# Optimization experiments

Measured on AMD Instinct MI355X. Metric: run time of the kernel, lower is better.

Reference implementation:

```python
import jax, jax.numpy as jnp
import numpy as np

NFEAT, NHID, NCLASS = 64, 64, 32
B, N_SOLUTE, N_SOLVENT = 2, 2076, 8940


def setup_inputs() -> dict:
    key = jax.random.key(0)
    ks = jax.random.split(key, 20)
    s = 0.05
    return {
        "solute_adj": jax.random.uniform(ks[0], (B, N_SOLUTE, N_SOLUTE), jnp.float32),
        "solute_meth": jax.random.normal(ks[1], (B, N_SOLUTE, NFEAT), jnp.float32),
        "solvent_meth": jax.random.normal(ks[2], (B, N_SOLVENT, NFEAT), jnp.float32),
        "solvent_adj_meth": jax.random.uniform(ks[3], (B, N_SOLVENT, N_SOLVENT), jnp.float32),
        "W_fc1": jax.random.normal(ks[4], (NFEAT, NCLASS), jnp.float32) * s,
        "b_fc1": jnp.zeros((NCLASS,), jnp.float32),
        "W_c1": jax.random.normal(ks[5], (NFEAT, NHID), jnp.float32) * s,
        "b_c1": jnp.zeros((NHID,), jnp.float32),
        "W_c2": jax.random.normal(ks[6], (NHID, NCLASS), jnp.float32) * s,
        "b_c2": jnp.zeros((NCLASS,), jnp.float32),
        "W_fc2": jax.random.normal(ks[7], (2 * NCLASS, NCLASS), jnp.float32) * s,
        "b_fc2": jnp.zeros((NCLASS,), jnp.float32),
        "W_fc3": jax.random.normal(ks[8], (NCLASS, 64), jnp.float32) * s,
        "b_fc3": jnp.zeros((64,), jnp.float32),
        "W_fc4": jax.random.normal(ks[9], (64, 32), jnp.float32) * s,
        "b_fc4": jnp.zeros((32,), jnp.float32),
        "W_fc5": jax.random.normal(ks[10], (32, 1), jnp.float32) * s,
        "b_fc5": jnp.zeros((1,), jnp.float32),
    }


def _branch(x, adj, W_fc1, b_fc1, W_c1, b_c1, W_c2, b_c2):
    # residual linear skip: fc1(x)
    init = x @ W_fc1 + b_fc1                          # [B, N, nclass]
    # GCNConv 1: adj @ (x W) + b, relu
    h = jax.nn.relu(jnp.einsum("bnm,bmh->bnh", adj, x @ W_c1) + b_c1)
    # GCNConv 2 + skip
    out = jnp.einsum("bnm,bmc->bnc", adj, h @ W_c2) + b_c2 + init  # [B, N, nclass]
    # global max pool: batch index is block-contiguous -> max over node axis
    return jnp.max(out, axis=1)                       # [B, nclass]


def reference(solute_adj, solute_meth, solvent_meth, solvent_adj_meth,
              W_fc1, b_fc1, W_c1, b_c1, W_c2, b_c2,
              W_fc2, b_fc2, W_fc3, b_fc3, W_fc4, b_fc4, W_fc5, b_fc5):
    su = _branch(solute_meth, solute_adj, W_fc1, b_fc1, W_c1, b_c1, W_c2, b_c2)
    sv = _branch(solvent_meth, solvent_adj_meth, W_fc1, b_fc1, W_c1, b_c1, W_c2, b_c2)
    d = jnp.concatenate([su, sv], axis=1)             # [B, 2*nclass]
    d = jax.nn.relu(d @ W_fc2 + b_fc2)                # dropout = identity (eval)
    d = jax.nn.relu(d @ W_fc3 + b_fc3)
    d = jax.nn.relu(d @ W_fc4 + b_fc4)
    return d @ W_fc5 + b_fc5                          # [B, 1]
```

## Files before the change

### kernel.cpp

```cpp
#include <hip/hip_runtime.h>

#define B_      2
#define NSU     2076
#define NSV     8940
#define ROWS_SU (B_ * NSU)
#define ROWS_ALL (B_ * (NSU + NSV))
#define MP_SU   2176
#define MP_SV   8960
#define NB64_SV 140
#define NB64_SU 33
#define NBX_TOT (2 * NB64_SV + 2 * NB64_SU)
#define NH1     5
#define NH2     8
#define KQ_SV   1792
#define KQ_SU   448
#define NCH_SV  140
#define NCH_SU  33
#define T_SV    560
#define T_SU    132
#define TILES_TOT (2 * T_SV + 2 * T_SU)
#define PADROWS (TILES_TOT * 16)
#define TSZ8_SV ((size_t)140 * 1024)
#define TSZ8_SU ((size_t)34 * 1024)
#define SU_BASE8 ((size_t)2 * T_SV * TSZ8_SV)
#define NEG_INF (-3.402823466e38f)

#define Y1F_SV(b) ((size_t)(b) * 140 * 4096)
#define Y1F_SU(b) ((size_t)2 * 140 * 4096 + (size_t)(b) * 34 * 4096)
#define Y2F8_SV(b) ((size_t)(b) * 140 * 2048)
#define Y2F8_SU(b) ((size_t)2 * 140 * 2048 + (size_t)(b) * 34 * 2048)

typedef __attribute__((ext_vector_type(8))) short bf16x8;
typedef __attribute__((ext_vector_type(4))) float f32x4;
typedef __attribute__((ext_vector_type(2))) long longx2;

union BF8 { bf16x8 v; unsigned int u[4]; };

#define MFMA16 __builtin_amdgcn_mfma_f32_16x16x32_bf16
#define MFMA8  __builtin_amdgcn_mfma_f32_16x16x32_fp8_fp8

__device__ __forceinline__ unsigned short f2bf(float x) {
    unsigned int u = __float_as_uint(x);
    u += 0x7FFFu + ((u >> 16) & 1u);
    return (unsigned short)(u >> 16);
}
__device__ __forceinline__ unsigned int pkbf(float lo, float hi) {
    unsigned int r;
    asm("v_cvt_pk_bf16_f32 %0, %1, %2" : "=v"(r) : "v"(lo), "v"(hi));
    return r;
}
__device__ __forceinline__ int pk8lo(float lo, float hi, int old) {
    return __builtin_amdgcn_cvt_pk_fp8_f32(lo, hi, old, false);
}
__device__ __forceinline__ int pk8hi(float lo, float hi, int old) {
    return __builtin_amdgcn_cvt_pk_fp8_f32(lo, hi, old, true);
}

__global__ __launch_bounds__(256) void pre_kernel(
    const float* __restrict__ xsu, const float* __restrict__ xsv,
    const float* __restrict__ Wc1, const float* __restrict__ Wfc1,
    const float* __restrict__ bfc1,
    unsigned short* __restrict__ y1tf, float* __restrict__ initb)
{
    __shared__ float sWc1[64 * 64];
    __shared__ float sWfc1[64 * 32];
    __shared__ float sb[32];
    const int tid = threadIdx.x;
    for (int i = tid; i < 64 * 64; i += 256) sWc1[i] = Wc1[i];
    for (int i = tid; i < 64 * 32; i += 256) sWfc1[i] = Wfc1[i];
    if (tid < 32) sb[tid] = bfc1[tid];
    __syncthreads();

    const int rid = blockIdx.x * 256 + tid;
    if (rid >= ROWS_ALL) return;

    const float* xrow; unsigned short* yb; int m;
    if (rid < ROWS_SU) {
        int b = rid / NSU; m = rid - b * NSU;
        xrow = xsu + (size_t)rid * 64;
        yb = y1tf + Y1F_SU(b);
    } else {
        int r2 = rid - ROWS_SU;
        int b = r2 / NSV; m = r2 - b * NSV;
        xrow = xsv + (size_t)r2 * 64;
        yb = y1tf + Y1F_SV(b);
    }

    float xr[64];
    #pragma unroll
    for (int f4 = 0; f4 < 16; ++f4) {
        float4 v = ((const float4*)xrow)[f4];
        xr[f4 * 4 + 0] = v.x; xr[f4 * 4 + 1] = v.y;
        xr[f4 * 4 + 2] = v.z; xr[f4 * 4 + 3] = v.w;
    }
    {
        const int chunk = m >> 6, half = (m >> 5) & 1, kqq = (m >> 3) & 3, e = m & 7;
        unsigned short* yw = yb + (size_t)chunk * 4096 + half * 512 + e;
        for (int c = 0; c < 64; ++c) {
            float acc = 0.f;
            #pragma unroll
            for (int f = 0; f < 64; ++f) acc += xr[f] * sWc1[f * 64 + c];
            yw[(c >> 4) * 1024 + ((c & 15) + 16 * kqq) * 8] = f2bf(acc);
        }
    }
    float* ini = initb + (size_t)rid * 32;
    for (int c = 0; c < 32; ++c) {
        float acc = sb[c];
        #pragma unroll
        for (int f = 0; f < 64; ++f) acc += xr[f] * sWfc1[f * 32 + c];
        ini[c] = acc;
    }
}

__global__ __launch_bounds__(256) void conv1p_kernel(
    const float* __restrict__ adj_su, const float* __restrict__ adj_sv,
    const unsigned short* __restrict__ y1tf,
    unsigned char* __restrict__ abf8,
    float* __restrict__ p1)
{
    const int bid = blockIdx.x;
    const int q = blockIdx.y;
    const int tid = threadIdx.x, lane = tid & 63, wid = tid >> 6;
    int M, row0, tile0, KQ;
    const float* A; const unsigned short* Yf; unsigned char* AbT;
    if (bid < 2 * NB64_SV) {
        int b = bid / NB64_SV, rb = bid - b * NB64_SV;
        M = NSV; KQ = KQ_SV;
        A  = adj_sv + (size_t)b * NSV * NSV;
        Yf = y1tf + Y1F_SV(b);
        row0 = rb * 64; tile0 = b * T_SV + rb * 4;
        AbT = abf8 + (size_t)(tile0 + wid) * TSZ8_SV;
    } else {
        int t = bid - 2 * NB64_SV;
        int b = t / NB64_SU, rb = t - b * NB64_SU;
        M = NSU; KQ = KQ_SU;
        A  = adj_su + (size_t)b * NSU * NSU;
        Yf = y1tf + Y1F_SU(b);
        row0 = rb * 64;
        int tsu = b * T_SU + rb * 4;
        tile0 = 2 * T_SV + tsu;
        AbT = abf8 + SU_BASE8 + (size_t)(tsu + wid) * TSZ8_SU;
    }
    const int kbeg = q * KQ;
    const int kend = (q == NH1 - 1) ? M : (kbeg + KQ);

    const int l15 = lane & 15, kq = lane >> 4;
    const int gr  = row0 + wid * 16 + l15;
    const int grc = (gr < M) ? gr : (M - 1);
    const float* Ap  = A + (size_t)grc * M;
    const float* Apk = Ap + kq * 8;
    const unsigned short* Bl = Yf + (size_t)lane * 8;

    f32x4 acc0 = {0.f,0.f,0.f,0.f}, acc1 = acc0, acc2 = acc0, acc3 = acc0;

    float4 a0,a1,a2,a3, c0,c1,c2,c3;
    bf16x8 b0,b1,b2,b3,b4,b5,b6,b7, d0,d1,d2,d3,d4,d5,d6,d7;

#define LDA(A0,A1,A2,A3,kc) do { \
    A0 = *(const float4*)(Apk + (kc)); \
    A1 = *(const float4*)(Apk + (kc) + 4); \
    A2 = *(const float4*)(Apk + (kc) + 32); \
    A3 = *(const float4*)(Apk + (kc) + 36); } while (0)
#define LDB(B0,B1,B2,B3,B4,B5,B6,B7,kc) do { \
    const unsigned short* bb = Bl + ((size_t)((kc) >> 6)) * 4096; \
    B0 = *(const bf16x8*)(bb); \
    B1 = *(const bf16x8*)(bb + 512); \
    B2 = *(const bf16x8*)(bb + 1024); \
    B3 = *(const bf16x8*)(bb + 1536); \
    B4 = *(const bf16x8*)(bb + 2048); \
    B5 = *(const bf16x8*)(bb + 2560); \
    B6 = *(const bf16x8*)(bb + 3072); \
    B7 = *(const bf16x8*)(bb + 3584); } while (0)
#define CVT(F0,F1,A0,A1,A2,A3) do { \
    F0.u[0] = pkbf(A0.x, A0.y); F0.u[1] = pkbf(A0.z, A0.w); \
    F0.u[2] = pkbf(A1.x, A1.y); F0.u[3] = pkbf(A1.z, A1.w); \
    F1.u[0] = pkbf(A2.x, A2.y); F1.u[1] = pkbf(A2.z, A2.w); \
    F1.u[2] = pkbf(A3.x, A3.y); F1.u[3] = pkbf(A3.z, A3.w); } while (0)
#define STF8(A0,A1,A2,A3,kc) do { \
    int q0 = pk8lo(A0.x, A0.y, 0); q0 = pk8hi(A0.z, A0.w, q0); \
    int q1 = pk8lo(A1.x, A1.y, 0); q1 = pk8hi(A1.z, A1.w, q1); \
    int q2 = pk8lo(A2.x, A2.y, 0); q2 = pk8hi(A2.z, A2.w, q2); \
    int q3 = pk8lo(A3.x, A3.y, 0); q3 = pk8hi(A3.z, A3.w, q3); \
    *(int4*)(AbT + ((size_t)((kc) >> 6)) * 1024 + lane * 16) = make_int4(q0, q1, q2, q3); } while (0)
#define CMP8(F0,F1,B0,B1,B2,B3,B4,B5,B6,B7) do { \
    acc0 = MFMA16(F0.v, B0, acc0, 0, 0, 0); \
    acc1 = MFMA16(F0.v, B2, acc1, 0, 0, 0); \
    acc2 = MFMA16(F0.v, B4, acc2, 0, 0, 0); \
    acc3 = MFMA16(F0.v, B6, acc3, 0, 0, 0); \
    acc0 = MFMA16(F1.v, B1, acc0, 0, 0, 0); \
    acc1 = MFMA16(F1.v, B3, acc1, 0, 0, 0); \
    acc2 = MFMA16(F1.v, B5, acc2, 0, 0, 0); \
    acc3 = MFMA16(F1.v, B7, acc3, 0, 0, 0); } while (0)

    const int klast = kbeg + ((kend - kbeg) & ~63);
    if (klast > kbeg) {
        LDA(a0,a1,a2,a3, kbeg);
        LDB(b0,b1,b2,b3,b4,b5,b6,b7, kbeg);
        int kc = kbeg;
        while (kc + 128 <= klast) {
            LDA(c0,c1,c2,c3, kc + 64);
            LDB(d0,d1,d2,d3,d4,d5,d6,d7, kc + 64);
            { BF8 f0, f1; CVT(f0,f1,a0,a1,a2,a3); STF8(a0,a1,a2,a3,kc);
              CMP8(f0,f1,b0,b1,b2,b3,b4,b5,b6,b7); }
            if (kc + 128 < klast) {
                LDA(a0,a1,a2,a3, kc + 128);
                LDB(b0,b1,b2,b3,b4,b5,b6,b7, kc + 128);
            }
            { BF8 f0, f1; CVT(f0,f1,c0,c1,c2,c3); STF8(c0,c1,c2,c3,kc + 64);
              CMP8(f0,f1,d0,d1,d2,d3,d4,d5,d6,d7); }
            kc += 128;
        }
        if (kc < klast) {
            BF8 f0, f1; CVT(f0,f1,a0,a1,a2,a3); STF8(a0,a1,a2,a3,kc);
            CMP8(f0,f1,b0,b1,b2,b3,b4,b5,b6,b7);
        }
    }
    if (klast < kend) {
        BF8 f0, f1;
        float xs[8], ys[8];
        #pragma unroll
        for (int e = 0; e < 8; ++e) {
            const int ka = klast + kq * 8 + e;
            xs[e] = (ka      < kend) ? Ap[ka]      : 0.f;
            ys[e] = (ka + 32 < kend) ? Ap[ka + 32] : 0.f;
        }
        #pragma unroll
        for (int e = 0; e < 8; e += 2) {
            f0.u[e >> 1] = pkbf(xs[e], xs[e + 1]);
            f1.u[e >> 1] = pkbf(ys[e], ys[e + 1]);
        }
        int q0 = pk8lo(xs[0], xs[1], 0); q0 = pk8hi(xs[2], xs[3], q0);
        int q1 = pk8lo(xs[4], xs[5], 0); q1 = pk8hi(xs[6], xs[7], q1);
        int q2 = pk8lo(ys[0], ys[1], 0); q2 = pk8hi(ys[2], ys[3], q2);
        int q3 = pk8lo(ys[4], ys[5], 0); q3 = pk8hi(ys[6], ys[7], q3);
        *(int4*)(AbT + ((size_t)(klast >> 6)) * 1024 + lane * 16) = make_int4(q0, q1, q2, q3);
        LDB(b0,b1,b2,b3,b4,b5,b6,b7, klast);
        CMP8(f0,f1,b0,b1,b2,b3,b4,b5,b6,b7);
    }
#undef LDA
#undef LDB
#undef CVT
#undef STF8
#undef CMP8

    float* Pp = p1 + ((size_t)q * TILES_TOT + tile0 + wid) * (16 * 64);
    #pragma unroll
    for (int j = 0; j < 4; ++j) {
        const int r = kq * 4 + j;
        Pp[r * 64 +      l15] = acc0[j];
        Pp[r * 64 + 16 + l15] = acc1[j];
        Pp[r * 64 + 32 + l15] = acc2[j];
        Pp[r * 64 + 48 + l15] = acc3[j];
    }
}

__global__ __launch_bounds__(256) void combine1_kernel(
    const float* __restrict__ p1, const float* __restrict__ bc1,
    const float* __restrict__ Wc2g, unsigned char* __restrict__ y2f8)
{
    __shared__ float sW[64][32];
    __shared__ float sb[64];
    const int tid = threadIdx.x;
    for (int i = tid; i < 2048; i += 256) sW[i >> 5][i & 31] = Wc2g[i];
    if (tid < 64) sb[tid] = bc1[tid];
    __syncthreads();

    const int pr = blockIdx.x * 64 + (tid & 63);
    const int cq = tid >> 6;
    int m, M; unsigned char* y2b;
    if (pr < 2 * T_SV * 16) {
        int b = pr / (T_SV * 16);
        m = pr - b * (T_SV * 16);
        M = NSV;
        y2b = y2f8 + Y2F8_SV(b);
    } else {
        int t = pr - 2 * T_SV * 16;
        int b = t / (T_SU * 16);
        m = t - b * (T_SU * 16);
        M = NSU;
        y2b = y2f8 + Y2F8_SU(b);
    }
    const float* P0 = p1 + (size_t)pr * 64;
    const float* P1 = P0 + (size_t)PADROWS * 64;
    const float* P2 = P1 + (size_t)PADROWS * 64;
    const float* P3 = P2 + (size_t)PADROWS * 64;
    const float* P4 = P3 + (size_t)PADROWS * 64;
    float h[64];
    #pragma unroll
    for (int f4 = 0; f4 < 16; ++f4) {
        float4 u = ((const float4*)P0)[f4];
        float4 v = ((const float4*)P1)[f4];
        float4 w = ((const float4*)P2)[f4];
        float4 z = ((const float4*)P3)[f4];
        float4 y = ((const float4*)P4)[f4];
        h[f4 * 4 + 0] = fmaxf(u.x + v.x + w.x + z.x + y.x + sb[f4 * 4 + 0], 0.f);
        h[f4 * 4 + 1] = fmaxf(u.y + v.y + w.y + z.y + y.y + sb[f4 * 4 + 1], 0.f);
        h[f4 * 4 + 2] = fmaxf(u.z + v.z + w.z + z.z + y.z + sb[f4 * 4 + 2], 0.f);
        h[f4 * 4 + 3] = fmaxf(u.w + v.w + w.w + z.w + y.w + sb[f4 * 4 + 3], 0.f);
    }
    float acc[8] = {0.f,0.f,0.f,0.f,0.f,0.f,0.f,0.f};
    #pragma unroll
    for (int f = 0; f < 64; ++f) {
        const float hv = h[f];
        const float4 w0 = *(const float4*)&sW[f][cq * 8];
        const float4 w1 = *(const float4*)&sW[f][cq * 8 + 4];
        acc[0] += hv * w0.x; acc[1] += hv * w0.y; acc[2] += hv * w0.z; acc[3] += hv * w0.w;
        acc[4] += hv * w1.x; acc[5] += hv * w1.y; acc[6] += hv * w1.z; acc[7] += hv * w1.w;
    }
    if (m < M) {
        const int chunk = m >> 6, half = (m >> 5) & 1, kqq = (m >> 3) & 3, e = m & 7;
        unsigned char* yw = y2b + (size_t)chunk * 2048 + half * 8 + e;
        #pragma unroll
        for (int j = 0; j < 8; ++j) {
            const int c = cq * 8 + j;
            const int pk = pk8lo(acc[j], acc[j], 0);
            yw[(c >> 4) * 1024 + (kqq * 16 + (c & 15)) * 16] = (unsigned char)(pk & 0xff);
        }
    }
}

__global__ __launch_bounds__(256) void conv2p_kernel(
    const unsigned char* __restrict__ abf8,
    const unsigned char* __restrict__ y2f8,
    float* __restrict__ p2)
{
    const int bid = (NBX_TOT - 1) - blockIdx.x;
    const int q = blockIdx.y;
    const int tid = threadIdx.x, lane = tid & 63, wid = tid >> 6;
    int tile0, cbeg, cend;
    const unsigned char* Yf2; const unsigned char* AbT;
    if (bid < 2 * NB64_SV) {
        int b = bid / NB64_SV, rb = bid - b * NB64_SV;
        Yf2 = y2f8 + Y2F8_SV(b);
        tile0 = b * T_SV + rb * 4;
        AbT = abf8 + (size_t)(tile0 + wid) * TSZ8_SV;
        cbeg = (q * NCH_SV) >> 3;
        cend = ((q + 1) * NCH_SV) >> 3;
    } else {
        int t = bid - 2 * NB64_SV;
        int b = t / NB64_SU, rb = t - b * NB64_SU;
        Yf2 = y2f8 + Y2F8_SU(b);
        int tsu = b * T_SU + rb * 4;
        tile0 = 2 * T_SV + tsu;
        AbT = abf8 + SU_BASE8 + (size_t)(tsu + wid) * TSZ8_SU;
        cbeg = (q * NCH_SU) >> 3;
        cend = ((q + 1) * NCH_SU) >> 3;
    }

    const int l15 = lane & 15, kq = lane >> 4;
    const unsigned char* Apl = AbT + (size_t)lane * 16;
    const unsigned char* Bpl = Yf2 + (size_t)lane * 16;

    f32x4 acc0 = {0.f,0.f,0.f,0.f}, acc1 = acc0;

    longx2 fa, fc;
    longx2 b0, b1, d0, d1;

#define LDA2(F, ch) do { F = *(const longx2*)(Apl + (size_t)(ch) * 1024); } while (0)
#define LDB2(B0,B1,ch) do { \
    const unsigned char* bb = Bpl + (size_t)(ch) * 2048; \
    B0 = *(const longx2*)(bb); \
    B1 = *(const longx2*)(bb + 1024); } while (0)
#define CMP4(F,B0,B1) do { \
    acc0 = MFMA8(F[0], B0[0], acc0, 0, 0, 0); \
    acc1 = MFMA8(F[0], B1[0], acc1, 0, 0, 0); \
    acc0 = MFMA8(F[1], B0[1], acc0, 0, 0, 0); \
    acc1 = MFMA8(F[1], B1[1], acc1, 0, 0, 0); } while (0)

    if (cbeg < cend) {
        LDA2(fa, cbeg);
        LDB2(b0, b1, cbeg);
        int ch = cbeg;
        while (ch + 2 <= cend) {
            LDA2(fc, ch + 1);
            LDB2(d0, d1, ch + 1);
            CMP4(fa, b0, b1);
            if (ch + 2 < cend) {
                LDA2(fa, ch + 2);
                LDB2(b0, b1, ch + 2);
            }
            CMP4(fc, d0, d1);
            ch += 2;
        }
        if (ch < cend) {
            CMP4(fa, b0, b1);
        }
    }
#undef LDA2
#undef LDB2
#undef CMP4

    float* Pp = p2 + ((size_t)q * TILES_TOT + tile0 + wid) * (16 * 32);
    #pragma unroll
    for (int j = 0; j < 4; ++j) {
        const int r = kq * 4 + j;
        Pp[r * 32 +      l15] = acc0[j];
        Pp[r * 32 + 16 + l15] = acc1[j];
    }
}

__global__ __launch_bounds__(256) void combine2_kernel(
    const float* __restrict__ p2, const float* __restrict__ bc2,
    const float* __restrict__ initb, float* __restrict__ part)
{
    const int idx = blockIdx.x * 256 + threadIdx.x;
    if (idx >= TILES_TOT * 32) return;
    const int gt = idx >> 5, c = idx & 31;
    int m0, M; const float* I;
    if (gt < 2 * T_SV) {
        int b = gt / T_SV;
        m0 = (gt - b * T_SV) * 16;
        M = NSV;
        I = initb + (size_t)ROWS_SU * 32 + (size_t)b * NSV * 32;
    } else {
        int t = gt - 2 * T_SV;
        int b = t / T_SU;
        m0 = (t - b * T_SU) * 16;
        M = NSU;
        I = initb + (size_t)b * NSU * 32;
    }
    const float* Q = p2 + (size_t)gt * 16 * 32 + c;
    const size_t QS = (size_t)TILES_TOT * 16 * 32;
    const float bb = bc2[c];
    float mx = NEG_INF;
    #pragma unroll
    for (int r = 0; r < 16; ++r) {
        const int m = m0 + r;
        if (m < M) {
            float s = bb + I[(size_t)m * 32 + c];
            #pragma unroll
            for (int qq = 0; qq < NH2; ++qq) s += Q[(size_t)qq * QS + r * 32];
            mx = fmaxf(mx, s);
        }
    }
    part[(size_t)gt * 32 + c] = mx;
}

__global__ __launch_bounds__(128) void head_kernel(
    const float* __restrict__ part,
    const float* __restrict__ Wfc2, const float* __restrict__ bfc2,
    const float* __restrict__ Wfc3, const float* __restrict__ bfc3,
    const float* __restrict__ Wfc4, const float* __restrict__ bfc4,
    const float* __restrict__ Wfc5, const float* __restrict__ bfc5,
    float* __restrict__ out)
{
    __shared__ float d[2][64];
    __shared__ float t1[2][32];
    __shared__ float t2[2][64];
    __shared__ float t3[2][32];
    const int tid = threadIdx.x;

    if (tid < 64) {
        const int b = tid >> 5, c = tid & 31;
        float m = NEG_INF;
        const float* ps = part + (size_t)(2 * T_SV + b * T_SU) * 32 + c;
        for (int i = 0; i < T_SU; ++i) m = fmaxf(m, ps[(size_t)i * 32]);
        d[b][c] = m;
        float m2 = NEG_INF;
        const float* pv = part + (size_t)b * T_SV * 32 + c;
        for (int i = 0; i < T_SV; ++i) m2 = fmaxf(m2, pv[(size_t)i * 32]);
        d[b][32 + c] = m2;
    }
    __syncthreads();
    if (tid < 64) {
        const int b = tid >> 5, c = tid & 31;
        float acc = bfc2[c];
        for (int f = 0; f < 64; ++f) acc += d[b][f] * Wfc2[f * 32 + c];
        t1[b][c] = fmaxf(acc, 0.f);
    }
    __syncthreads();
    {
        const int b = tid >> 6, c = tid & 63;
        float acc = bfc3[c];
        for (int f = 0; f < 32; ++f) acc += t1[b][f] * Wfc3[f * 64 + c];
        t2[b][c] = fmaxf(acc, 0.f);
    }
    __syncthreads();
    if (tid < 64) {
        const int b = tid >> 5, c = tid & 31;
        float acc = bfc4[c];
        for (int f = 0; f < 64; ++f) acc += t2[b][f] * Wfc4[f * 32 + c];
        t3[b][c] = fmaxf(acc, 0.f);
    }
    __syncthreads();
    if (tid < 2) {
        float acc = bfc5[0];
        for (int f = 0; f < 32; ++f) acc += t3[tid][f] * Wfc5[f];
        out[tid] = acc;
    }
}

extern "C" void kernel_launch(void* const* d_in, const int* in_sizes, int n_in,
                              void* d_out, int out_size, void* d_ws, size_t ws_size,
                              hipStream_t stream)
{
    const float* solute_adj   = (const float*)d_in[0];
    const float* solute_meth  = (const float*)d_in[1];
    const float* solvent_meth = (const float*)d_in[2];
    const float* solvent_adj  = (const float*)d_in[3];
    const float* W_fc1 = (const float*)d_in[4];
    const float* b_fc1 = (const float*)d_in[5];
    const float* W_c1  = (const float*)d_in[6];
    const float* b_c1  = (const float*)d_in[7];
    const float* W_c2  = (const float*)d_in[8];
    const float* b_c2  = (const float*)d_in[9];
    const float* W_fc2 = (const float*)d_in[10];
    const float* b_fc2 = (const float*)d_in[11];
    const float* W_fc3 = (const float*)d_in[12];
    const float* b_fc3 = (const float*)d_in[13];
    const float* W_fc4 = (const float*)d_in[14];
    const float* b_fc4 = (const float*)d_in[15];
    const float* W_fc5 = (const float*)d_in[16];
    const float* b_fc5 = (const float*)d_in[17];
    float* out = (float*)d_out;

    char* wsb = (char*)d_ws;
    size_t off = 0;
    unsigned short* y1tf = (unsigned short*)(wsb + off); off += 2850816;
    unsigned char*  y2f8 = (unsigned char*)(wsb + off);  off += 712704;
    off = (off + 15) & ~(size_t)15;
    float* initb         = (float*)(wsb + off);          off += 2820096;
    unsigned char* abf8  = (unsigned char*)(wsb + off);
    off += SU_BASE8 + (size_t)2 * T_SU * TSZ8_SU;
    off = (off + 15) & ~(size_t)15;
    float* p1            = (float*)(wsb + off);
    float* p2            = p1;
    off += (size_t)NH1 * PADROWS * 64 * 4;
    float* part          = (float*)(wsb + off);          off += (size_t)TILES_TOT * 32 * 4;

    pre_kernel<<<dim3((ROWS_ALL + 255) / 256), dim3(256), 0, stream>>>(
        solute_meth, solvent_meth, W_c1, W_fc1, b_fc1, y1tf, initb);

    conv1p_kernel<<<dim3(NBX_TOT, NH1), dim3(256), 0, stream>>>(
        solute_adj, solvent_adj, y1tf, abf8, p1);

    combine1_kernel<<<dim3(PADROWS / 64), dim3(256), 0, stream>>>(p1, b_c1, W_c2, y2f8);

    conv2p_kernel<<<dim3(NBX_TOT, NH2), dim3(256), 0, stream>>>(abf8, y2f8, p2);

    combine2_kernel<<<dim3((TILES_TOT * 32 + 255) / 256), dim3(256), 0, stream>>>(
        p2, b_c2, initb, part);

    head_kernel<<<dim3(1), dim3(128), 0, stream>>>(
        part, W_fc2, b_fc2, W_fc3, b_fc3, W_fc4, b_fc4, W_fc5, b_fc5, out);
}
```

Baseline: 471.8 us.

## Fuse conv1 with bias/relu and W_c2 projection, dropping split-K partials

Replaces the split-K conv1 kernel and its separate combine kernel with one kernel per 16-row tile. Each block streams the full K range of the fp32 adjacency through swizzled LDS as bf16, writes the fp8 adjacency copy, and then applies bias, ReLU and the W_c2 projection with MFMA before writing y2 in fp8. A transposed bf16 copy of W_c2 is produced by one extra block in pre_kernel. This removes the fp32 partial buffer round trip and one launch, but each block now covers only 16 rows with a single accumulator and syncs through LDS twice per 256-column chunk, so memory-level parallelism per block is lower than in the old split-K form.

```diff
diff --git a/kernel.cpp b/kernel.cpp
--- a/kernel.cpp
+++ b/kernel.cpp
@@ -5,17 +5,14 @@
 #define NSV     8940
 #define ROWS_SU (B_ * NSU)
 #define ROWS_ALL (B_ * (NSU + NSV))
-#define MP_SU   2176
-#define MP_SV   8960
 #define NB64_SV 140
 #define NB64_SU 33
 #define NBX_TOT (2 * NB64_SV + 2 * NB64_SU)
-#define NH1     5
 #define NH2     8
-#define KQ_SV   1792
-#define KQ_SU   448
 #define NCH_SV  140
 #define NCH_SU  33
+#define TK_SV   140
+#define TK_SU   33
 #define T_SV    560
 #define T_SU    132
 #define TILES_TOT (2 * T_SV + 2 * T_SU)
@@ -23,6 +20,7 @@
 #define TSZ8_SV ((size_t)140 * 1024)
 #define TSZ8_SU ((size_t)34 * 1024)
 #define SU_BASE8 ((size_t)2 * T_SV * TSZ8_SV)
+#define PRE_BLKS ((ROWS_ALL + 255) / 256)
 #define NEG_INF (-3.402823466e38f)
 
 #define Y1F_SV(b) ((size_t)(b) * 140 * 4096)
@@ -34,8 +32,6 @@
 typedef __attribute__((ext_vector_type(4))) float f32x4;
 typedef __attribute__((ext_vector_type(2))) long longx2;
 
-union BF8 { bf16x8 v; unsigned int u[4]; };
-
 #define MFMA16 __builtin_amdgcn_mfma_f32_16x16x32_bf16
 #define MFMA8  __builtin_amdgcn_mfma_f32_16x16x32_fp8_fp8
 
@@ -55,17 +51,29 @@
 __device__ __forceinline__ int pk8hi(float lo, float hi, int old) {
     return __builtin_amdgcn_cvt_pk_fp8_f32(lo, hi, old, true);
 }
+__device__ __forceinline__ float bf2f(short s) {
+    return __uint_as_float(((unsigned int)(unsigned short)s) << 16);
+}
 
 __global__ __launch_bounds__(256) void pre_kernel(
     const float* __restrict__ xsu, const float* __restrict__ xsv,
     const float* __restrict__ Wc1, const float* __restrict__ Wfc1,
-    const float* __restrict__ bfc1,
-    unsigned short* __restrict__ y1tf, float* __restrict__ initb)
-{
+    const float* __restrict__ bfc1, const float* __restrict__ Wc2g,
+    unsigned short* __restrict__ y1tf, float* __restrict__ initb,
+    unsigned short* __restrict__ wc2t)
+{
+    const int tid = threadIdx.x;
+    if (blockIdx.x == PRE_BLKS) {
+        for (int idx = tid; idx < 2048; idx += 256) {
+            const int c = idx >> 6, f = idx & 63;
+            wc2t[idx] = f2bf(Wc2g[f * 32 + c]);
+        }
+        return;
+    }
+
     __shared__ float sWc1[64 * 64];
     __shared__ float sWfc1[64 * 32];
     __shared__ float sb[32];
-    const int tid = threadIdx.x;
     for (int i = tid; i < 64 * 64; i += 256) sWc1[i] = Wc1[i];
     for (int i = tid; i < 64 * 32; i += 256) sWfc1[i] = Wfc1[i];
     if (tid < 32) sb[tid] = bfc1[tid];
@@ -112,210 +120,122 @@
     }
 }
 
-__global__ __launch_bounds__(256) void conv1p_kernel(
+__global__ __launch_bounds__(256) void conv1f_kernel(
     const float* __restrict__ adj_su, const float* __restrict__ adj_sv,
     const unsigned short* __restrict__ y1tf,
+    const float* __restrict__ bc1, const unsigned short* __restrict__ wc2t,
     unsigned char* __restrict__ abf8,
-    float* __restrict__ p1)
-{
-    const int bid = blockIdx.x;
-    const int q = blockIdx.y;
-    const int tid = threadIdx.x, lane = tid & 63, wid = tid >> 6;
-    int M, row0, tile0, KQ;
-    const float* A; const unsigned short* Yf; unsigned char* AbT;
-    if (bid < 2 * NB64_SV) {
-        int b = bid / NB64_SV, rb = bid - b * NB64_SV;
-        M = NSV; KQ = KQ_SV;
-        A  = adj_sv + (size_t)b * NSV * NSV;
+    unsigned char* __restrict__ y2f8)
+{
+    __shared__ unsigned short AL[4096];
+    __shared__ unsigned short HL[1024];
+
+    const int t = blockIdx.x;
+    const int tid = threadIdx.x, lane = tid & 63, w = tid >> 6;
+    const int l15 = lane & 15, kq = lane >> 4;
+
+    int M, row0, TK;
+    const float* A; const unsigned short* Yf;
+    unsigned char* AbT; unsigned char* Y2b;
+    if (t < 2 * T_SV) {
+        int b = t / T_SV, rt = t - b * T_SV;
+        M = NSV; TK = TK_SV;
+        A = adj_sv + (size_t)b * NSV * NSV;
         Yf = y1tf + Y1F_SV(b);
-        row0 = rb * 64; tile0 = b * T_SV + rb * 4;
-        AbT = abf8 + (size_t)(tile0 + wid) * TSZ8_SV;
+        AbT = abf8 + (size_t)t * TSZ8_SV;
+        Y2b = y2f8 + Y2F8_SV(b);
+        row0 = rt * 16;
     } else {
-        int t = bid - 2 * NB64_SV;
-        int b = t / NB64_SU, rb = t - b * NB64_SU;
-        M = NSU; KQ = KQ_SU;
-        A  = adj_su + (size_t)b * NSU * NSU;
+        int u = t - 2 * T_SV;
+        int b = u / T_SU, rt = u - b * T_SU;
+        M = NSU; TK = TK_SU;
+        A = adj_su + (size_t)b * NSU * NSU;
         Yf = y1tf + Y1F_SU(b);
-        row0 = rb * 64;
-        int tsu = b * T_SU + rb * 4;
-        tile0 = 2 * T_SV + tsu;
-        AbT = abf8 + SU_BASE8 + (size_t)(tsu + wid) * TSZ8_SU;
-    }
-    const int kbeg = q * KQ;
-    const int kend = (q == NH1 - 1) ? M : (kbeg + KQ);
-
-    const int l15 = lane & 15, kq = lane >> 4;
-    const int gr  = row0 + wid * 16 + l15;
-    const int grc = (gr < M) ? gr : (M - 1);
-    const float* Ap  = A + (size_t)grc * M;
-    const float* Apk = Ap + kq * 8;
-    const unsigned short* Bl = Yf + (size_t)lane * 8;
-
-    f32x4 acc0 = {0.f,0.f,0.f,0.f}, acc1 = acc0, acc2 = acc0, acc3 = acc0;
-
-    float4 a0,a1,a2,a3, c0,c1,c2,c3;
-    bf16x8 b0,b1,b2,b3,b4,b5,b6,b7, d0,d1,d2,d3,d4,d5,d6,d7;
-
-#define LDA(A0,A1,A2,A3,kc) do { \
-    A0 = *(const float4*)(Apk + (kc)); \
-    A1 = *(const float4*)(Apk + (kc) + 4); \
-    A2 = *(const float4*)(Apk + (kc) + 32); \
-    A3 = *(const float4*)(Apk + (kc) + 36); } while (0)
-#define LDB(B0,B1,B2,B3,B4,B5,B6,B7,kc) do { \
-    const unsigned short* bb = Bl + ((size_t)((kc) >> 6)) * 4096; \
-    B0 = *(const bf16x8*)(bb); \
-    B1 = *(const bf16x8*)(bb + 512); \
-    B2 = *(const bf16x8*)(bb + 1024); \
-    B3 = *(const bf16x8*)(bb + 1536); \
-    B4 = *(const bf16x8*)(bb + 2048); \
-    B5 = *(const bf16x8*)(bb + 2560); \
-    B6 = *(const bf16x8*)(bb + 3072); \
-    B7 = *(const bf16x8*)(bb + 3584); } while (0)
-#define CVT(F0,F1,A0,A1,A2,A3) do { \
-    F0.u[0] = pkbf(A0.x, A0.y); F0.u[1] = pkbf(A0.z, A0.w); \
-    F0.u[2] = pkbf(A1.x, A1.y); F0.u[3] = pkbf(A1.z, A1.w); \
-    F1.u[0] = pkbf(A2.x, A2.y); F1.u[1] = pkbf(A2.z, A2.w); \
-    F1.u[2] = pkbf(A3.x, A3.y); F1.u[3] = pkbf(A3.z, A3.w); } while (0)
-#define STF8(A0,A1,A2,A3,kc) do { \
-    int q0 = pk8lo(A0.x, A0.y, 0); q0 = pk8hi(A0.z, A0.w, q0); \
-    int q1 = pk8lo(A1.x, A1.y, 0); q1 = pk8hi(A1.z, A1.w, q1); \
-    int q2 = pk8lo(A2.x, A2.y, 0); q2 = pk8hi(A2.z, A2.w, q2); \
-    int q3 = pk8lo(A3.x, A3.y, 0); q3 = pk8hi(A3.z, A3.w, q3); \
-    *(int4*)(AbT + ((size_t)((kc) >> 6)) * 1024 + lane * 16) = make_int4(q0, q1, q2, q3); } while (0)
-#define CMP8(F0,F1,B0,B1,B2,B3,B4,B5,B6,B7) do { \
-    acc0 = MFMA16(F0.v, B0, acc0, 0, 0, 0); \
-    acc1 = MFMA16(F0.v, B2, acc1, 0, 0, 0); \
-    acc2 = MFMA16(F0.v, B4, acc2, 0, 0, 0); \
-    acc3 = MFMA16(F0.v, B6, acc3, 0, 0, 0); \
-    acc0 = MFMA16(F1.v, B1, acc0, 0, 0, 0); \
-    acc1 = MFMA16(F1.v, B3, acc1, 0, 0, 0); \
-    acc2 = MFMA16(F1.v, B5, acc2, 0, 0, 0); \
-    acc3 = MFMA16(F1.v, B7, acc3, 0, 0, 0); } while (0)
-
-    const int klast = kbeg + ((kend - kbeg) & ~63);
-    if (klast > kbeg) {
-        LDA(a0,a1,a2,a3, kbeg);
-        LDB(b0,b1,b2,b3,b4,b5,b6,b7, kbeg);
-        int kc = kbeg;
-        while (kc + 128 <= klast) {
-            LDA(c0,c1,c2,c3, kc + 64);
-            LDB(d0,d1,d2,d3,d4,d5,d6,d7, kc + 64);
-            { BF8 f0, f1; CVT(f0,f1,a0,a1,a2,a3); STF8(a0,a1,a2,a3,kc);
-              CMP8(f0,f1,b0,b1,b2,b3,b4,b5,b6,b7); }
-            if (kc + 128 < klast) {
-                LDA(a0,a1,a2,a3, kc + 128);
-                LDB(b0,b1,b2,b3,b4,b5,b6,b7, kc + 128);
+        AbT = abf8 + SU_BASE8 + (size_t)u * TSZ8_SU;
+        Y2b = y2f8 + Y2F8_SU(b);
+        row0 = rt * 16;
+    }
+
+    const float* Ar[4];
+    #pragma unroll
+    for (int rr = 0; rr < 4; ++rr) {
+        int r = row0 + w * 4 + rr;
+        if (r >= M) r = M - 1;
+        Ar[rr] = A + (size_t)r * M;
+    }
+
+    const int c4 = lane * 4;
+    const int k64i = c4 >> 6;
+    const int c63 = c4 & 63;
+    const int rxor = (l15 & 7) << 3;
+
+    f32x4 acc = {0.f, 0.f, 0.f, 0.f};
+
+    for (int ch = 0; ch < TK; ch += 4) {
+        const int cb = ch * 64;
+        const int nk = (TK - ch < 4) ? (TK - ch) : 4;
+        #pragma unroll
+        for (int rr = 0; rr < 4; ++rr) {
+            const int r = w * 4 + rr;
+            const int col = cb + c4;
+            float4 v = make_float4(0.f, 0.f, 0.f, 0.f);
+            if (col < M) v = *(const float4*)(Ar[rr] + col);
+            const unsigned int u0 = pkbf(v.x, v.y);
+            const unsigned int u1 = pkbf(v.z, v.w);
+            const int sa = k64i * 1024 + r * 64 + (c63 ^ ((r & 7) << 3));
+            *(uint2*)(&AL[sa]) = make_uint2(u0, u1);
+        }
+        __syncthreads();
+        #pragma unroll
+        for (int j = 0; j < 4; ++j) {
+            if (j < nk) {
+                const bf16x8 af0 = *(const bf16x8*)(&AL[j * 1024 + l15 * 64 + ((kq * 8) ^ rxor)]);
+                const bf16x8 af1 = *(const bf16x8*)(&AL[j * 1024 + l15 * 64 + ((32 + kq * 8) ^ rxor)]);
+                const unsigned short* bb = Yf + (size_t)(ch + j) * 4096 + w * 1024 + lane * 8;
+                const bf16x8 b0 = *(const bf16x8*)(bb);
+                const bf16x8 b1 = *(const bf16x8*)(bb + 512);
+                acc = MFMA16(af0, b0, acc, 0, 0, 0);
+                acc = MFMA16(af1, b1, acc, 0, 0, 0);
             }
-            { BF8 f0, f1; CVT(f0,f1,c0,c1,c2,c3); STF8(c0,c1,c2,c3,kc + 64);
-              CMP8(f0,f1,d0,d1,d2,d3,d4,d5,d6,d7); }
-            kc += 128;
-        }
-        if (kc < klast) {
-            BF8 f0, f1; CVT(f0,f1,a0,a1,a2,a3); STF8(a0,a1,a2,a3,kc);
-            CMP8(f0,f1,b0,b1,b2,b3,b4,b5,b6,b7);
-        }
-    }
-    if (klast < kend) {
-        BF8 f0, f1;
-        float xs[8], ys[8];
+        }
+        if (w < nk) {
+            const bf16x8 h0 = *(const bf16x8*)(&AL[w * 1024 + l15 * 64 + ((kq * 8) ^ rxor)]);
+            const bf16x8 h1 = *(const bf16x8*)(&AL[w * 1024 + l15 * 64 + ((32 + kq * 8) ^ rxor)]);
+            int q0 = pk8lo(bf2f(h0[0]), bf2f(h0[1]), 0); q0 = pk8hi(bf2f(h0[2]), bf2f(h0[3]), q0);
+            int q1 = pk8lo(bf2f(h0[4]), bf2f(h0[5]), 0); q1 = pk8hi(bf2f(h0[6]), bf2f(h0[7]), q1);
+            int q2 = pk8lo(bf2f(h1[0]), bf2f(h1[1]), 0); q2 = pk8hi(bf2f(h1[2]), bf2f(h1[3]), q2);
+            int q3 = pk8lo(bf2f(h1[4]), bf2f(h1[5]), 0); q3 = pk8hi(bf2f(h1[6]), bf2f(h1[7]), q3);
+            *(int4*)(AbT + (size_t)(ch + w) * 1024 + lane * 16) = make_int4(q0, q1, q2, q3);
+        }
+        __syncthreads();
+    }
+
+    {
+        const float bcv = bc1[w * 16 + l15];
         #pragma unroll
-        for (int e = 0; e < 8; ++e) {
-            const int ka = klast + kq * 8 + e;
-            xs[e] = (ka      < kend) ? Ap[ka]      : 0.f;
-            ys[e] = (ka + 32 < kend) ? Ap[ka + 32] : 0.f;
-        }
-        #pragma unroll
-        for (int e = 0; e < 8; e += 2) {
-            f0.u[e >> 1] = pkbf(xs[e], xs[e + 1]);
-            f1.u[e >> 1] = pkbf(ys[e], ys[e + 1]);
-        }
-        int q0 = pk8lo(xs[0], xs[1], 0); q0 = pk8hi(xs[2], xs[3], q0);
-        int q1 = pk8lo(xs[4], xs[5], 0); q1 = pk8hi(xs[6], xs[7], q1);
-        int q2 = pk8lo(ys[0], ys[1], 0); q2 = pk8hi(ys[2], ys[3], q2);
-        int q3 = pk8lo(ys[4], ys[5], 0); q3 = pk8hi(ys[6], ys[7], q3);
-        *(int4*)(AbT + ((size_t)(klast >> 6)) * 1024 + lane * 16) = make_int4(q0, q1, q2, q3);
-        LDB(b0,b1,b2,b3,b4,b5,b6,b7, klast);
-        CMP8(f0,f1,b0,b1,b2,b3,b4,b5,b6,b7);
-    }
-#undef LDA
-#undef LDB
-#undef CVT
-#undef STF8
-#undef CMP8
-
-    float* Pp = p1 + ((size_t)q * TILES_TOT + tile0 + wid) * (16 * 64);
-    #pragma unroll
-    for (int j = 0; j < 4; ++j) {
-        const int r = kq * 4 + j;
-        Pp[r * 64 +      l15] = acc0[j];
-        Pp[r * 64 + 16 + l15] = acc1[j];
-        Pp[r * 64 + 32 + l15] = acc2[j];
-        Pp[r * 64 + 48 + l15] = acc3[j];
-    }
-}
-
-__global__ __launch_bounds__(256) void combine1_kernel(
-    const float* __restrict__ p1, const float* __restrict__ bc1,
-    const float* __restrict__ Wc2g, unsigned char* __restrict__ y2f8)
-{
-    __shared__ float sW[64][32];
-    __shared__ float sb[64];
-    const int tid = threadIdx.x;
-    for (int i = tid; i < 2048; i += 256) sW[i >> 5][i & 31] = Wc2g[i];
-    if (tid < 64) sb[tid] = bc1[tid];
-    __syncthreads();
-
-    const int pr = blockIdx.x * 64 + (tid & 63);
-    const int cq = tid >> 6;
-    int m, M; unsigned char* y2b;
-    if (pr < 2 * T_SV * 16) {
-        int b = pr / (T_SV * 16);
-        m = pr - b * (T_SV * 16);
-        M = NSV;
-        y2b = y2f8 + Y2F8_SV(b);
-    } else {
-        int t = pr - 2 * T_SV * 16;
-        int b = t / (T_SU * 16);
-        m = t - b * (T_SU * 16);
-        M = NSU;
-        y2b = y2f8 + Y2F8_SU(b);
-    }
-    const float* P0 = p1 + (size_t)pr * 64;
-    const float* P1 = P0 + (size_t)PADROWS * 64;
-    const float* P2 = P1 + (size_t)PADROWS * 64;
-    const float* P3 = P2 + (size_t)PADROWS * 64;
-    const float* P4 = P3 + (size_t)PADROWS * 64;
-    float h[64];
-    #pragma unroll
-    for (int f4 = 0; f4 < 16; ++f4) {
-        float4 u = ((const float4*)P0)[f4];
-        float4 v = ((const float4*)P1)[f4];
-        float4 w = ((const float4*)P2)[f4];
-        float4 z = ((const float4*)P3)[f4];
-        float4 y = ((const float4*)P4)[f4];
-        h[f4 * 4 + 0] = fmaxf(u.x + v.x + w.x + z.x + y.x + sb[f4 * 4 + 0], 0.f);
-        h[f4 * 4 + 1] = fmaxf(u.y + v.y + w.y + z.y + y.y + sb[f4 * 4 + 1], 0.f);
-        h[f4 * 4 + 2] = fmaxf(u.z + v.z + w.z + z.z + y.z + sb[f4 * 4 + 2], 0.f);
-        h[f4 * 4 + 3] = fmaxf(u.w + v.w + w.w + z.w + y.w + sb[f4 * 4 + 3], 0.f);
-    }
-    float acc[8] = {0.f,0.f,0.f,0.f,0.f,0.f,0.f,0.f};
-    #pragma unroll
-    for (int f = 0; f < 64; ++f) {
-        const float hv = h[f];
-        const float4 w0 = *(const float4*)&sW[f][cq * 8];
-        const float4 w1 = *(const float4*)&sW[f][cq * 8 + 4];
-        acc[0] += hv * w0.x; acc[1] += hv * w0.y; acc[2] += hv * w0.z; acc[3] += hv * w0.w;
-        acc[4] += hv * w1.x; acc[5] += hv * w1.y; acc[6] += hv * w1.z; acc[7] += hv * w1.w;
-    }
-    if (m < M) {
-        const int chunk = m >> 6, half = (m >> 5) & 1, kqq = (m >> 3) & 3, e = m & 7;
-        unsigned char* yw = y2b + (size_t)chunk * 2048 + half * 8 + e;
-        #pragma unroll
-        for (int j = 0; j < 8; ++j) {
-            const int c = cq * 8 + j;
-            const int pk = pk8lo(acc[j], acc[j], 0);
-            yw[(c >> 4) * 1024 + (kqq * 16 + (c & 15)) * 16] = (unsigned char)(pk & 0xff);
-        }
+        for (int j = 0; j < 4; ++j) {
+            const int r = kq * 4 + j;
+            const int c = w * 16 + l15;
+            HL[r * 64 + (c ^ ((r & 7) << 3))] = f2bf(fmaxf(acc[j] + bcv, 0.f));
+        }
+    }
+    __syncthreads();
+    if (w < 2) {
+        const bf16x8 hf0 = *(const bf16x8*)(&HL[l15 * 64 + ((kq * 8) ^ rxor)]);
+        const bf16x8 hf1 = *(const bf16x8*)(&HL[l15 * 64 + ((32 + kq * 8) ^ rxor)]);
+        const unsigned short* wp = wc2t + (size_t)(w * 16 + l15) * 64 + kq * 8;
+        const bf16x8 w0 = *(const bf16x8*)(wp);
+        const bf16x8 w1 = *(const bf16x8*)(wp + 32);
+        f32x4 m = {0.f, 0.f, 0.f, 0.f};
+        m = MFMA16(hf0, w0, m, 0, 0, 0);
+        m = MFMA16(hf1, w1, m, 0, 0, 0);
+        const int mrow = row0 + kq * 4;
+        const int chm = mrow >> 6, r6 = mrow & 63;
+        const int halfm = r6 >> 5, kqqm = (r6 >> 3) & 3, e0 = r6 & 7;
+        const int c = w * 16 + l15;
+        int pk = pk8lo(m[0], m[1], 0); pk = pk8hi(m[2], m[3], pk);
+        *(int*)(Y2b + (size_t)chm * 2048 + (c >> 4) * 1024
+                + (kqqm * 16 + (c & 15)) * 16 + halfm * 8 + e0) = pk;
     }
 }
 
@@ -518,23 +438,20 @@
     size_t off = 0;
     unsigned short* y1tf = (unsigned short*)(wsb + off); off += 2850816;
     unsigned char*  y2f8 = (unsigned char*)(wsb + off);  off += 712704;
-    off = (off + 15) & ~(size_t)15;
+    unsigned short* wc2t = (unsigned short*)(wsb + off); off += 4096;
     float* initb         = (float*)(wsb + off);          off += 2820096;
     unsigned char* abf8  = (unsigned char*)(wsb + off);
     off += SU_BASE8 + (size_t)2 * T_SU * TSZ8_SU;
     off = (off + 15) & ~(size_t)15;
-    float* p1            = (float*)(wsb + off);
-    float* p2            = p1;
-    off += (size_t)NH1 * PADROWS * 64 * 4;
+    float* p2            = (float*)(wsb + off);
+    off += (size_t)NH2 * PADROWS * 32 * 4;
     float* part          = (float*)(wsb + off);          off += (size_t)TILES_TOT * 32 * 4;
 
-    pre_kernel<<<dim3((ROWS_ALL + 255) / 256), dim3(256), 0, stream>>>(
-        solute_meth, solvent_meth, W_c1, W_fc1, b_fc1, y1tf, initb);
-
-    conv1p_kernel<<<dim3(NBX_TOT, NH1), dim3(256), 0, stream>>>(
-        solute_adj, solvent_adj, y1tf, abf8, p1);
-
-    combine1_kernel<<<dim3(PADROWS / 64), dim3(256), 0, stream>>>(p1, b_c1, W_c2, y2f8);
+    pre_kernel<<<dim3(PRE_BLKS + 1), dim3(256), 0, stream>>>(
+        solute_meth, solvent_meth, W_c1, W_fc1, b_fc1, W_c2, y1tf, initb, wc2t);
+
+    conv1f_kernel<<<dim3(TILES_TOT), dim3(256), 0, stream>>>(
+        solute_adj, solvent_adj, y1tf, b_c1, wc2t, abf8, y2f8);
 
     conv2p_kernel<<<dim3(NBX_TOT, NH2), dim3(256), 0, stream>>>(abf8, y2f8, p2);
 
```

Measured after the change: 440.8 us. 6.6% less time.
